# Kernel tuning notes

Measured on AMD Instinct MI355X. Metric: run time of the kernel, lower is better.

The kernel has to match this reference:

```python
import jax, jax.numpy as jnp
import numpy as np

NUM_HEADS = 1  # the module's reshape only type-checks for num_heads == 1 (see notes)


def setup_inputs() -> dict:
    key = jax.random.key(0)
    ks = jax.random.split(key, 9)
    B, S, H = 16, 4096, 512
    std = 0.02
    return {
        "x": jax.random.normal(ks[0], (B, S, H), dtype=jnp.float32),
        "Wq": jax.random.normal(ks[1], (H, H), dtype=jnp.float32) * std,
        "bq": jnp.zeros((H,), dtype=jnp.float32),
        "Wk": jax.random.normal(ks[2], (H, H), dtype=jnp.float32) * std,
        "bk": jnp.zeros((H,), dtype=jnp.float32),
        "Wv": jax.random.normal(ks[3], (H, H), dtype=jnp.float32) * std,
        "bv": jnp.zeros((H,), dtype=jnp.float32),
        "Wo": jax.random.normal(ks[4], (H, H), dtype=jnp.float32) * std,
        "bo": jnp.zeros((H,), dtype=jnp.float32),
    }


def reference(x, Wq, bq, Wk, bk, Wv, bv, Wo, bo):
    B, S, H = x.shape
    nh = NUM_HEADS
    hd = H // nh
    # Faithful to the torch code: view(B*nh, S, hd).transpose(1, 2) -> (G, hd, S)
    q = (x @ Wq + bq).reshape(B * nh, S, hd).transpose(0, 2, 1)  # (G, hd, S)
    k = (x @ Wk + bk).reshape(B * nh, S, hd).transpose(0, 2, 1)  # (G, hd, S)
    v = (x @ Wv + bv).reshape(B * nh, S, hd).transpose(0, 2, 1)  # (G, hd, S)
    # Attention matrix is over feature dims: (G, hd, hd), contraction over S
    scores = jnp.einsum('gds,ges->gde', q, k) / jnp.sqrt(jnp.float32(hd))
    attn = jax.nn.softmax(scores, axis=-1)                        # (G, hd, hd)
    attn_out = jnp.einsum('gde,ges->gds', attn, v)                # (G, hd, S)
    attn_out = attn_out.transpose(0, 2, 1)                        # (G, S, hd) == (B, S, H) for nh=1
    return attn_out @ Wo + bo
```

## Files before the change

kernel.cpp:

```cpp
#include <hip/hip_runtime.h>
#include <hip/hip_bf16.h>


typedef __attribute__((ext_vector_type(4))) float f32x4;
typedef __attribute__((ext_vector_type(8))) __bf16 bf16x8;
typedef __attribute__((ext_vector_type(4))) __bf16 bf16x4;

typedef __attribute__((address_space(1))) const void gconst_void;
typedef __attribute__((address_space(3))) void lds_void;

__device__ __forceinline__ void gload_lds16(const void* g, void* l) {
  __builtin_amdgcn_global_load_lds((gconst_void*)g, (lds_void*)l, 16, 0, 0);
}

__device__ __forceinline__ void cvt_hilo(float v, __bf16& h, __bf16& l) {
  h = (__bf16)v;
  l = (__bf16)(v - (float)h);
}

template <int MODE, int BMN>
__global__ __launch_bounds__(256) void gemm3p(
    const void* Ap, const void* ApLo,
    const void* Bp, const void* BpLo,
    float* __restrict__ C,
    int M, int N, int K,
    long long sAg, long long sBg, long long sCg,
    const float* bias, long long sBiasG,
    float alpha, int tri, int splitK)
{
  constexpr int LD = (MODE == 1) ? 64 : 72;
  constexpr int R = BMN / 32;
  __shared__ __align__(16) __bf16 sAhi[BMN * LD];
  __shared__ __align__(16) __bf16 sAlo[BMN * LD];
  __shared__ __align__(16) __bf16 sBhi[BMN * LD];
  __shared__ __align__(16) __bf16 sBlo[BMN * LD];

  const int t = threadIdx.x;
  const int g = blockIdx.z;
  int m0, n0, kBeg, kEnd;
  if (tri) {
    int p = blockIdx.x, bx = 0;
    while ((bx + 1) * (bx + 2) / 2 <= p) ++bx;
    int by = p - bx * (bx + 1) / 2;
    m0 = bx * BMN; n0 = by * BMN;
    int kLen = K / splitK;
    kBeg = blockIdx.y * kLen; kEnd = kBeg + kLen;
  } else {
    m0 = blockIdx.y * BMN; n0 = blockIdx.x * BMN;
    kBeg = 0; kEnd = K;
  }
  const int lane = t & 63;
  const int w = t >> 6, wm = w >> 1, wn = w & 1;
  const int lr = lane & 15, lg = lane >> 4;

  const f32x4 fzero = {0.f, 0.f, 0.f, 0.f};
  f32x4 acc[R][R];
#pragma unroll
  for (int i = 0; i < R; ++i)
#pragma unroll
    for (int j = 0; j < R; ++j) acc[i][j] = fzero;

  for (int k0 = kBeg; k0 < kEnd; k0 += 64) {
    __syncthreads();
    if constexpr (MODE == 1) {
      const __bf16* Ah = (const __bf16*)Ap + g * sAg;
      const __bf16* Al = (const __bf16*)ApLo + g * sAg;
      const __bf16* Bh = (const __bf16*)Bp + g * sBg;
      const __bf16* Bl = (const __bf16*)BpLo + g * sBg;
#pragma unroll
      for (int it = 0; it < BMN / 32; ++it) {
        int r = it * 32 + (t >> 3);
        int sl = (t & 7) ^ (r & 7);
        long long ea = (long long)(m0 + r) * K + k0 + sl * 8;
        long long eb = (long long)(n0 + r) * K + k0 + sl * 8;
        int dst = it * 4096 + (t >> 6) * 1024;
        gload_lds16(Ah + ea, (char*)sAhi + dst);
        gload_lds16(Al + ea, (char*)sAlo + dst);
        gload_lds16(Bh + eb, (char*)sBhi + dst);
        gload_lds16(Bl + eb, (char*)sBlo + dst);
      }
    } else {
      const float* A = (const float*)Ap + g * sAg;
      const float* B = (const float*)Bp + g * sBg;
      const int f = t & 15, r0 = t >> 4;
#pragma unroll
      for (int p = 0; p < BMN / 16; ++p) {
        int r = r0 + p * 16;
        float4 va = *(const float4*)(A + (long long)(m0 + r) * K + k0 + f * 4);
        float4 vb = *(const float4*)(B + (long long)(n0 + r) * K + k0 + f * 4);
        bf16x4 ah4, al4, bh4, bl4;
        __bf16 hh, ll;
        cvt_hilo(va.x, hh, ll); ah4[0] = hh; al4[0] = ll;
        cvt_hilo(va.y, hh, ll); ah4[1] = hh; al4[1] = ll;
        cvt_hilo(va.z, hh, ll); ah4[2] = hh; al4[2] = ll;
        cvt_hilo(va.w, hh, ll); ah4[3] = hh; al4[3] = ll;
        cvt_hilo(vb.x, hh, ll); bh4[0] = hh; bl4[0] = ll;
        cvt_hilo(vb.y, hh, ll); bh4[1] = hh; bl4[1] = ll;
        cvt_hilo(vb.z, hh, ll); bh4[2] = hh; bl4[2] = ll;
        cvt_hilo(vb.w, hh, ll); bh4[3] = hh; bl4[3] = ll;
        *(bf16x4*)&sAhi[r * LD + f * 4] = ah4;
        *(bf16x4*)&sAlo[r * LD + f * 4] = al4;
        *(bf16x4*)&sBhi[r * LD + f * 4] = bh4;
        *(bf16x4*)&sBlo[r * LD + f * 4] = bl4;
      }
    }
    __syncthreads();
#pragma unroll
    for (int ks = 0; ks < 2; ++ks) {
      bf16x8 ah[R], al[R], bh[R], bl[R];
#pragma unroll
      for (int i = 0; i < R; ++i) {
        int ra = wm * (BMN / 2) + i * 16 + lr;
        int rb = wn * (BMN / 2) + i * 16 + lr;
        int oa, ob;
        if constexpr (MODE == 1) {
          oa = ra * 64 + (((ks * 4 + lg) ^ (ra & 7)) * 8);
          ob = rb * 64 + (((ks * 4 + lg) ^ (rb & 7)) * 8);
        } else {
          oa = ra * LD + ks * 32 + lg * 8;
          ob = rb * LD + ks * 32 + lg * 8;
        }
        ah[i] = *(const bf16x8*)&sAhi[oa];
        al[i] = *(const bf16x8*)&sAlo[oa];
        bh[i] = *(const bf16x8*)&sBhi[ob];
        bl[i] = *(const bf16x8*)&sBlo[ob];
      }
#pragma unroll
      for (int i = 0; i < R; ++i)
#pragma unroll
        for (int j = 0; j < R; ++j) {
          acc[i][j] = __builtin_amdgcn_mfma_f32_16x16x32_bf16(ah[i], bh[j], acc[i][j], 0, 0, 0);
          acc[i][j] = __builtin_amdgcn_mfma_f32_16x16x32_bf16(ah[i], bl[j], acc[i][j], 0, 0, 0);
          acc[i][j] = __builtin_amdgcn_mfma_f32_16x16x32_bf16(al[i], bh[j], acc[i][j], 0, 0, 0);
        }
    }
  }

  float* Cg = C + g * sCg;
  const float* bg = bias ? bias + g * sBiasG : nullptr;
#pragma unroll
  for (int i = 0; i < R; ++i) {
    int row = m0 + wm * (BMN / 2) + i * 16 + lg * 4;
#pragma unroll
    for (int j = 0; j < R; ++j) {
      int col = n0 + wn * (BMN / 2) + j * 16 + lr;
      if (splitK > 1) {
#pragma unroll
        for (int q = 0; q < 4; ++q)
          atomicAdd(&Cg[(long long)(row + q) * N + col], acc[i][j][q] * alpha);
      } else {
        float bb = bg ? bg[col] : 0.0f;
#pragma unroll
        for (int q = 0; q < 4; ++q)
          Cg[(long long)(row + q) * N + col] = acc[i][j][q] * alpha + bb;
      }
    }
  }
}

__global__ __launch_bounds__(256) void transcvt_k(
    const float* __restrict__ x, __bf16* __restrict__ xTh, __bf16* __restrict__ xTl,
    float* __restrict__ ssum)
{
  __shared__ float tile[64][65];
  const int g = blockIdx.z, h0 = blockIdx.x * 64, s0 = blockIdx.y * 64;
  const int t = threadIdx.x, f = t & 15, r0 = t >> 4;
#pragma unroll
  for (int p = 0; p < 4; ++p) {
    int r = r0 + p * 16;
    float4 v = *(const float4*)(x + ((long long)g * 4096 + s0 + r) * 512 + h0 + f * 4);
    tile[f * 4 + 0][r] = v.x;
    tile[f * 4 + 1][r] = v.y;
    tile[f * 4 + 2][r] = v.z;
    tile[f * 4 + 3][r] = v.w;
  }
  __syncthreads();
  const int hr = t >> 2, sc = t & 3;
  long long ob = ((long long)g * 512 + h0 + hr) * 4096 + s0 + sc * 16;
  float csum = 0.f;
#pragma unroll
  for (int i4 = 0; i4 < 4; ++i4) {
    bf16x4 hv, lv;
#pragma unroll
    for (int q = 0; q < 4; ++q) {
      float vv = tile[hr][sc * 16 + i4 * 4 + q];
      csum += vv;
      __bf16 hh, ll;
      cvt_hilo(vv, hh, ll);
      hv[q] = hh; lv[q] = ll;
    }
    *(bf16x4*)(xTh + ob + i4 * 4) = hv;
    *(bf16x4*)(xTl + ob + i4 * 4) = lv;
  }
  csum += __shfl_xor(csum, 1);
  csum += __shfl_xor(csum, 2);
  if ((t & 3) == 0) atomicAdd(&ssum[g * 512 + h0 + hr], csum);
}

__global__ __launch_bounds__(256) void transp_k(
    const float* __restrict__ src, float* __restrict__ dst,
    int M, int N, long long sg, long long sgT, int triOnly)
{
  __shared__ float tile[64][65];
  const int g = blockIdx.z, n0 = blockIdx.x * 64, m0 = blockIdx.y * 64;
  if (triOnly && m0 <= n0) return;
  const int t = threadIdx.x, f = t & 15, r0 = t >> 4;
  const float* s = src + g * sg;
  float* d = dst + g * sgT;
#pragma unroll
  for (int p = 0; p < 4; ++p) {
    int r = r0 + p * 16;
    float4 v = *(const float4*)(s + (long long)(m0 + r) * N + n0 + f * 4);
    tile[f * 4 + 0][r] = v.x;
    tile[f * 4 + 1][r] = v.y;
    tile[f * 4 + 2][r] = v.z;
    tile[f * 4 + 3][r] = v.w;
  }
  __syncthreads();
  const int nr = t >> 2, mc = t & 3;
#pragma unroll
  for (int i4 = 0; i4 < 4; ++i4) {
    float4 o;
    o.x = tile[nr][mc * 16 + i4 * 4 + 0];
    o.y = tile[nr][mc * 16 + i4 * 4 + 1];
    o.z = tile[nr][mc * 16 + i4 * 4 + 2];
    o.w = tile[nr][mc * 16 + i4 * 4 + 3];
    *(float4*)(d + (long long)(n0 + nr) * M + m0 + mc * 16 + i4 * 4) = o;
  }
}

__global__ __launch_bounds__(256) void wtrans_k(
    const float* __restrict__ Wq, const float* __restrict__ Wk, const float* __restrict__ Wo,
    float* __restrict__ WqT, float* __restrict__ WkT, float* __restrict__ WoT)
{
  __shared__ float tile[64][65];
  const int z = blockIdx.z;
  const float* s = (z == 0) ? Wq : (z == 1) ? Wk : Wo;
  float* d = (z == 0) ? WqT : (z == 1) ? WkT : WoT;
  const int n0 = blockIdx.x * 64, m0 = blockIdx.y * 64;
  const int t = threadIdx.x, f = t & 15, r0 = t >> 4;
#pragma unroll
  for (int p = 0; p < 4; ++p) {
    int r = r0 + p * 16;
    float4 v = *(const float4*)(s + (long long)(m0 + r) * 512 + n0 + f * 4);
    tile[f * 4 + 0][r] = v.x;
    tile[f * 4 + 1][r] = v.y;
    tile[f * 4 + 2][r] = v.z;
    tile[f * 4 + 3][r] = v.w;
  }
  __syncthreads();
  const int nr = t >> 2, mc = t & 3;
#pragma unroll
  for (int i4 = 0; i4 < 4; ++i4) {
    float4 o;
    o.x = tile[nr][mc * 16 + i4 * 4 + 0];
    o.y = tile[nr][mc * 16 + i4 * 4 + 1];
    o.z = tile[nr][mc * 16 + i4 * 4 + 2];
    o.w = tile[nr][mc * 16 + i4 * 4 + 3];
    *(float4*)(d + (long long)(n0 + nr) * 512 + m0 + mc * 16 + i4 * 4) = o;
  }
}

__global__ __launch_bounds__(256) void cvt32_k(
    const float* __restrict__ src, __bf16* __restrict__ h, __bf16* __restrict__ l,
    long long n4)
{
  long long stride = (long long)gridDim.x * 256;
  for (long long i = blockIdx.x * 256LL + threadIdx.x; i < n4; i += stride) {
    float4 v = ((const float4*)src)[i];
    bf16x4 hv, lv;
    __bf16 hh, ll;
    cvt_hilo(v.x, hh, ll); hv[0] = hh; lv[0] = ll;
    cvt_hilo(v.y, hh, ll); hv[1] = hh; lv[1] = ll;
    cvt_hilo(v.z, hh, ll); hv[2] = hh; lv[2] = ll;
    cvt_hilo(v.w, hh, ll); hv[3] = hh; lv[3] = ll;
    *(bf16x4*)(h + i * 4) = hv;
    *(bf16x4*)(l + i * 4) = lv;
  }
}

__global__ __launch_bounds__(256) void rk_k(
    const float* __restrict__ ssum, const float* __restrict__ Wq, const float* __restrict__ Wk,
    float* __restrict__ rho, float* __restrict__ kap)
{
  const int g = blockIdx.y, d = blockIdx.x * 256 + threadIdx.x;
  float r = 0.f, k = 0.f;
  for (int f = 0; f < 512; ++f) {
    float s = ssum[g * 512 + f];
    r += s * Wq[f * 512 + d];
    k += s * Wk[f * 512 + d];
  }
  rho[g * 512 + d] = r;
  kap[g * 512 + d] = k;
}

__global__ __launch_bounds__(256) void softmax_k(
    float* __restrict__ SC, const float* __restrict__ rho, const float* __restrict__ kap,
    const float* __restrict__ bq, const float* __restrict__ bk, float alpha)
{
  const int rowid = blockIdx.x * 4 + (threadIdx.x >> 6);
  const int g = rowid >> 9, d = rowid & 511;
  const int l = threadIdx.x & 63;
  float* row = SC + (long long)rowid * 512;
  const float bqd = bq[d];
  const float rr = rho[g * 512 + d] + 4096.f * bqd;
  float4 z0 = *(float4*)(row + l * 8);
  float4 z1 = *(float4*)(row + l * 8 + 4);
  float4 bk0 = *(const float4*)(bk + l * 8);
  float4 bk1 = *(const float4*)(bk + l * 8 + 4);
  float4 kp0 = *(const float4*)(kap + g * 512 + l * 8);
  float4 kp1 = *(const float4*)(kap + g * 512 + l * 8 + 4);
  float z[8];
  z[0] = z0.x + alpha * (bqd * kp0.x + bk0.x * rr);
  z[1] = z0.y + alpha * (bqd * kp0.y + bk0.y * rr);
  z[2] = z0.z + alpha * (bqd * kp0.z + bk0.z * rr);
  z[3] = z0.w + alpha * (bqd * kp0.w + bk0.w * rr);
  z[4] = z1.x + alpha * (bqd * kp1.x + bk1.x * rr);
  z[5] = z1.y + alpha * (bqd * kp1.y + bk1.y * rr);
  z[6] = z1.z + alpha * (bqd * kp1.z + bk1.z * rr);
  z[7] = z1.w + alpha * (bqd * kp1.w + bk1.w * rr);
  float m = z[0];
#pragma unroll
  for (int j = 1; j < 8; ++j) m = fmaxf(m, z[j]);
  for (int o = 32; o; o >>= 1) m = fmaxf(m, __shfl_xor(m, o));
  float sum = 0.f;
#pragma unroll
  for (int j = 0; j < 8; ++j) { z[j] = __expf(z[j] - m); sum += z[j]; }
  for (int o = 32; o; o >>= 1) sum += __shfl_xor(sum, o);
  const float inv = 1.0f / sum;
  *(float4*)(row + l * 8)     = make_float4(z[0] * inv, z[1] * inv, z[2] * inv, z[3] * inv);
  *(float4*)(row + l * 8 + 4) = make_float4(z[4] * inv, z[5] * inv, z[6] * inv, z[7] * inv);
}

__global__ __launch_bounds__(256) void cvec_k(
    const float* __restrict__ Aat, const float* __restrict__ bv, const float* __restrict__ bo,
    float* __restrict__ c)
{
  const int g = blockIdx.z, h = blockIdx.x * 256 + threadIdx.x, eb = blockIdx.y;
  float p = (eb == 0) ? bo[h] : 0.f;
  for (int e = eb * 64; e < eb * 64 + 64; ++e)
    p += bv[e] * Aat[((long long)g * 512 + e) * 512 + h];
  atomicAdd(&c[g * 512 + h], p);
}

extern "C" void kernel_launch(void* const* d_in, const int* in_sizes, int n_in,
                              void* d_out, int out_size, void* d_ws, size_t ws_size,
                              hipStream_t stream) {
  (void)in_sizes; (void)n_in; (void)out_size; (void)ws_size;
  const float* x  = (const float*)d_in[0];
  const float* Wq = (const float*)d_in[1];
  const float* bq = (const float*)d_in[2];
  const float* Wk = (const float*)d_in[3];
  const float* bk = (const float*)d_in[4];
  const float* Wv = (const float*)d_in[5];
  const float* bv = (const float*)d_in[6];
  const float* Wo = (const float*)d_in[7];
  const float* bo = (const float*)d_in[8];
  float* out = (float*)d_out;

  char* ws = (char*)d_ws;
  __bf16* xTh = (__bf16*)(ws);
  __bf16* xTl = (__bf16*)(ws + 67108864);
  float* S1   = (float*)(ws + 134217728);
  float* S2   = (float*)(ws + 150994944);
  float* S3   = (float*)(ws + 167772160);
  float* WqT  = (float*)(ws + 184549376);
  float* WkT  = (float*)(ws + 185597952);
  float* WoT  = (float*)(ws + 186646528);
  float* ssum = (float*)(ws + 187695104);
  float* cbuf = (float*)(ws + 187695104 + 32768);
  float* rho  = (float*)(ws + 187695104 + 65536);
  float* kap  = (float*)(ws + 187695104 + 98304);

  __bf16* PThi = (__bf16*)S2;
  __bf16* PTlo = (__bf16*)((char*)S2 + 8388608);
  __bf16* xnh = xTh;
  __bf16* xnl = xTl;

  const long long SXT = 512LL * 4096;
  const long long SM  = 512LL * 512;
  const long long SX  = 4096LL * 512;
  const float alpha = 0.04419417382415922f;

  hipMemsetAsync(ssum, 0, 65536, stream);
  hipMemsetAsync(S1, 0, 16777216, stream);

  transcvt_k<<<dim3(8, 64, 16), 256, 0, stream>>>(x, xTh, xTl, ssum);
  wtrans_k<<<dim3(8, 8, 3), 256, 0, stream>>>(Wq, Wk, Wo, WqT, WkT, WoT);
  rk_k<<<dim3(2, 16), 256, 0, stream>>>(ssum, Wq, Wk, rho, kap);

  gemm3p<1, 128><<<dim3(10, 4, 16), 256, 0, stream>>>(
      xTh, xTl, xTh, xTl, S1, 512, 512, 4096, SXT, SXT, SM, nullptr, 0, 1.0f, 1, 4);
  transp_k<<<dim3(8, 8, 16), 256, 0, stream>>>(S1, S1, 512, 512, SM, SM, 1);

  gemm3p<0, 64><<<dim3(8, 8, 16), 256, 0, stream>>>(
      WkT, nullptr, S1, nullptr, S2, 512, 512, 512, 0, SM, SM, nullptr, 0, 1.0f, 0, 1);
  gemm3p<0, 64><<<dim3(8, 8, 16), 256, 0, stream>>>(
      WqT, nullptr, S2, nullptr, S3, 512, 512, 512, 0, SM, SM, nullptr, 0, alpha, 0, 1);
  softmax_k<<<2048, 256, 0, stream>>>(S3, rho, kap, bq, bk, alpha);
  transp_k<<<dim3(8, 8, 16), 256, 0, stream>>>(S3, S1, 512, 512, SM, SM, 0);
  gemm3p<0, 64><<<dim3(8, 8, 16), 256, 0, stream>>>(
      S1, nullptr, WoT, nullptr, S2, 512, 512, 512, SM, 0, SM, nullptr, 0, 1.0f, 0, 1);
  cvec_k<<<dim3(2, 8, 16), 256, 0, stream>>>(S2, bv, bo, cbuf);
  transp_k<<<dim3(8, 8, 16), 256, 0, stream>>>(S2, S3, 512, 512, SM, SM, 0);
  gemm3p<0, 64><<<dim3(8, 8, 16), 256, 0, stream>>>(
      S3, nullptr, Wv, nullptr, S1, 512, 512, 512, SM, 0, SM, nullptr, 0, 1.0f, 0, 1);

  cvt32_k<<<2048, 256, 0, stream>>>(S1, PThi, PTlo, 16LL * 512 * 512 / 4);
  cvt32_k<<<2048, 256, 0, stream>>>(x, xnh, xnl, 16LL * 4096 * 512 / 4);

  gemm3p<1, 128><<<dim3(4, 32, 16), 256, 0, stream>>>(
      xnh, xnl, PThi, PTlo, out, 4096, 512, 512, SX, SM, SX, cbuf, 512, 1.0f, 0, 1);
}
```

Measured before the change: 717.3 us.

## Fuse conversions, transposes and bias vector into neighbouring kernels; shrink MODE1 K-tile

```diff
diff --git a/kernel.cpp b/kernel.cpp
--- a/kernel.cpp
+++ b/kernel.cpp
@@ -22,18 +22,22 @@
 __global__ __launch_bounds__(256) void gemm3p(
     const void* Ap, const void* ApLo,
     const void* Bp, const void* BpLo,
-    float* __restrict__ C,
+    float* __restrict__ C, __bf16* __restrict__ Cbh, __bf16* __restrict__ Cbl,
     int M, int N, int K,
     long long sAg, long long sBg, long long sCg,
     const float* bias, long long sBiasG,
-    float alpha, int tri, int splitK)
-{
-  constexpr int LD = (MODE == 1) ? 64 : 72;
+    float alpha, int tri, int splitK, int tepi)
+{
+  constexpr int LD = (MODE == 1) ? 32 : 72;
+  constexpr int BK = (MODE == 1) ? 32 : 64;
+  constexpr int KS = BK / 32;
   constexpr int R = BMN / 32;
-  __shared__ __align__(16) __bf16 sAhi[BMN * LD];
-  __shared__ __align__(16) __bf16 sAlo[BMN * LD];
-  __shared__ __align__(16) __bf16 sBhi[BMN * LD];
-  __shared__ __align__(16) __bf16 sBlo[BMN * LD];
+  __shared__ __align__(16) char smem[4 * BMN * LD * 2];
+  __bf16* sAhi = (__bf16*)smem;
+  __bf16* sAlo = sAhi + BMN * LD;
+  __bf16* sBhi = sAlo + BMN * LD;
+  __bf16* sBlo = sBhi + BMN * LD;
+  float* tpose = (float*)smem;
 
   const int t = threadIdx.x;
   const int g = blockIdx.z;
@@ -60,7 +64,7 @@
 #pragma unroll
     for (int j = 0; j < R; ++j) acc[i][j] = fzero;
 
-  for (int k0 = kBeg; k0 < kEnd; k0 += 64) {
+  for (int k0 = kBeg; k0 < kEnd; k0 += BK) {
     __syncthreads();
     if constexpr (MODE == 1) {
       const __bf16* Ah = (const __bf16*)Ap + g * sAg;
@@ -68,12 +72,12 @@
       const __bf16* Bh = (const __bf16*)Bp + g * sBg;
       const __bf16* Bl = (const __bf16*)BpLo + g * sBg;
 #pragma unroll
-      for (int it = 0; it < BMN / 32; ++it) {
-        int r = it * 32 + (t >> 3);
-        int sl = (t & 7) ^ (r & 7);
+      for (int half = 0; half < 2; ++half) {
+        int r = half * 64 + (t >> 2);
+        int sl = (t & 3) ^ (r & 3);
         long long ea = (long long)(m0 + r) * K + k0 + sl * 8;
         long long eb = (long long)(n0 + r) * K + k0 + sl * 8;
-        int dst = it * 4096 + (t >> 6) * 1024;
+        int dst = half * 4096 + (t >> 6) * 1024;
         gload_lds16(Ah + ea, (char*)sAhi + dst);
         gload_lds16(Al + ea, (char*)sAlo + dst);
         gload_lds16(Bh + eb, (char*)sBhi + dst);
@@ -106,7 +110,7 @@
     }
     __syncthreads();
 #pragma unroll
-    for (int ks = 0; ks < 2; ++ks) {
+    for (int ks = 0; ks < KS; ++ks) {
       bf16x8 ah[R], al[R], bh[R], bl[R];
 #pragma unroll
       for (int i = 0; i < R; ++i) {
@@ -114,8 +118,8 @@
         int rb = wn * (BMN / 2) + i * 16 + lr;
         int oa, ob;
         if constexpr (MODE == 1) {
-          oa = ra * 64 + (((ks * 4 + lg) ^ (ra & 7)) * 8);
-          ob = rb * 64 + (((ks * 4 + lg) ^ (rb & 7)) * 8);
+          oa = ra * 32 + ((lg ^ (ra & 3)) * 8);
+          ob = rb * 32 + ((lg ^ (rb & 3)) * 8);
         } else {
           oa = ra * LD + ks * 32 + lg * 8;
           ob = rb * LD + ks * 32 + lg * 8;
@@ -136,6 +140,55 @@
     }
   }
 
+  if (tepi) {
+    __syncthreads();
+#pragma unroll
+    for (int i = 0; i < R; ++i) {
+      int rowl = wm * (BMN / 2) + i * 16 + lg * 4;
+#pragma unroll
+      for (int j = 0; j < R; ++j) {
+        int coll = wn * (BMN / 2) + j * 16 + lr;
+#pragma unroll
+        for (int q = 0; q < 4; ++q)
+          tpose[(rowl + q) * 65 + coll] = acc[i][j][q] * alpha;
+      }
+    }
+    __syncthreads();
+    float* Cg = C + g * sCg;
+    const int nr = t >> 2, mc = t & 3;
+#pragma unroll
+    for (int i4 = 0; i4 < 4; ++i4) {
+      float4 o;
+      o.x = tpose[(mc * 16 + i4 * 4 + 0) * 65 + nr];
+      o.y = tpose[(mc * 16 + i4 * 4 + 1) * 65 + nr];
+      o.z = tpose[(mc * 16 + i4 * 4 + 2) * 65 + nr];
+      o.w = tpose[(mc * 16 + i4 * 4 + 3) * 65 + nr];
+      *(float4*)&Cg[(long long)(n0 + nr) * M + m0 + mc * 16 + i4 * 4] = o;
+    }
+    return;
+  }
+
+  if (Cbh) {
+    __bf16* Ch = Cbh + g * sCg;
+    __bf16* Cl2 = Cbl + g * sCg;
+#pragma unroll
+    for (int i = 0; i < R; ++i) {
+      int row = m0 + wm * (BMN / 2) + i * 16 + lg * 4;
+#pragma unroll
+      for (int j = 0; j < R; ++j) {
+        int col = n0 + wn * (BMN / 2) + j * 16 + lr;
+#pragma unroll
+        for (int q = 0; q < 4; ++q) {
+          __bf16 hh, ll;
+          cvt_hilo(acc[i][j][q] * alpha, hh, ll);
+          Ch[(long long)(row + q) * N + col] = hh;
+          Cl2[(long long)(row + q) * N + col] = ll;
+        }
+      }
+    }
+    return;
+  }
+
   float* Cg = C + g * sCg;
   const float* bg = bias ? bias + g * sBiasG : nullptr;
 #pragma unroll
@@ -160,7 +213,7 @@
 
 __global__ __launch_bounds__(256) void transcvt_k(
     const float* __restrict__ x, __bf16* __restrict__ xTh, __bf16* __restrict__ xTl,
-    float* __restrict__ ssum)
+    __bf16* __restrict__ xh, __bf16* __restrict__ xl, float* __restrict__ ssum)
 {
   __shared__ float tile[64][65];
   const int g = blockIdx.z, h0 = blockIdx.x * 64, s0 = blockIdx.y * 64;
@@ -168,7 +221,18 @@
 #pragma unroll
   for (int p = 0; p < 4; ++p) {
     int r = r0 + p * 16;
-    float4 v = *(const float4*)(x + ((long long)g * 4096 + s0 + r) * 512 + h0 + f * 4);
+    long long ib = ((long long)g * 4096 + s0 + r) * 512 + h0 + f * 4;
+    float4 v = *(const float4*)(x + ib);
+    if (xh) {
+      bf16x4 hv, lv;
+      __bf16 hh, ll;
+      cvt_hilo(v.x, hh, ll); hv[0] = hh; lv[0] = ll;
+      cvt_hilo(v.y, hh, ll); hv[1] = hh; lv[1] = ll;
+      cvt_hilo(v.z, hh, ll); hv[2] = hh; lv[2] = ll;
+      cvt_hilo(v.w, hh, ll); hv[3] = hh; lv[3] = ll;
+      *(bf16x4*)(xh + ib) = hv;
+      *(bf16x4*)(xl + ib) = lv;
+    }
     tile[f * 4 + 0][r] = v.x;
     tile[f * 4 + 1][r] = v.y;
     tile[f * 4 + 2][r] = v.z;
@@ -296,7 +360,8 @@
 
 __global__ __launch_bounds__(256) void softmax_k(
     float* __restrict__ SC, const float* __restrict__ rho, const float* __restrict__ kap,
-    const float* __restrict__ bq, const float* __restrict__ bk, float alpha)
+    const float* __restrict__ bq, const float* __restrict__ bk, const float* __restrict__ bv,
+    float* __restrict__ avb, float alpha)
 {
   const int rowid = blockIdx.x * 4 + (threadIdx.x >> 6);
   const int g = rowid >> 9, d = rowid & 511;
@@ -330,23 +395,28 @@
   const float inv = 1.0f / sum;
   *(float4*)(row + l * 8)     = make_float4(z[0] * inv, z[1] * inv, z[2] * inv, z[3] * inv);
   *(float4*)(row + l * 8 + 4) = make_float4(z[4] * inv, z[5] * inv, z[6] * inv, z[7] * inv);
-}
-
-__global__ __launch_bounds__(256) void cvec_k(
-    const float* __restrict__ Aat, const float* __restrict__ bv, const float* __restrict__ bo,
+  float4 bv0 = *(const float4*)(bv + l * 8);
+  float4 bv1 = *(const float4*)(bv + l * 8 + 4);
+  float av = z[0] * bv0.x + z[1] * bv0.y + z[2] * bv0.z + z[3] * bv0.w +
+             z[4] * bv1.x + z[5] * bv1.y + z[6] * bv1.z + z[7] * bv1.w;
+  for (int o = 32; o; o >>= 1) av += __shfl_xor(av, o);
+  if (l == 0) avb[g * 512 + d] = av * inv;
+}
+
+__global__ __launch_bounds__(256) void cvec2_k(
+    const float* __restrict__ avb, const float* __restrict__ Wo, const float* __restrict__ bo,
     float* __restrict__ c)
 {
-  const int g = blockIdx.z, h = blockIdx.x * 256 + threadIdx.x, eb = blockIdx.y;
-  float p = (eb == 0) ? bo[h] : 0.f;
-  for (int e = eb * 64; e < eb * 64 + 64; ++e)
-    p += bv[e] * Aat[((long long)g * 512 + e) * 512 + h];
-  atomicAdd(&c[g * 512 + h], p);
+  const int g = blockIdx.y, h = blockIdx.x * 256 + threadIdx.x;
+  float p = bo[h];
+  for (int d = 0; d < 512; ++d) p += avb[g * 512 + d] * Wo[d * 512 + h];
+  c[g * 512 + h] = p;
 }
 
 extern "C" void kernel_launch(void* const* d_in, const int* in_sizes, int n_in,
                               void* d_out, int out_size, void* d_ws, size_t ws_size,
                               hipStream_t stream) {
-  (void)in_sizes; (void)n_in; (void)out_size; (void)ws_size;
+  (void)in_sizes; (void)n_in; (void)out_size;
   const float* x  = (const float*)d_in[0];
   const float* Wq = (const float*)d_in[1];
   const float* bq = (const float*)d_in[2];
@@ -359,56 +429,78 @@
   float* out = (float*)d_out;
 
   char* ws = (char*)d_ws;
-  __bf16* xTh = (__bf16*)(ws);
-  __bf16* xTl = (__bf16*)(ws + 67108864);
-  float* S1   = (float*)(ws + 134217728);
-  float* S2   = (float*)(ws + 150994944);
-  float* S3   = (float*)(ws + 167772160);
-  float* WqT  = (float*)(ws + 184549376);
-  float* WkT  = (float*)(ws + 185597952);
-  float* WoT  = (float*)(ws + 186646528);
-  float* ssum = (float*)(ws + 187695104);
-  float* cbuf = (float*)(ws + 187695104 + 32768);
-  float* rho  = (float*)(ws + 187695104 + 65536);
-  float* kap  = (float*)(ws + 187695104 + 98304);
+  const long long MB = 1048576;
+  const bool big = ws_size >= (size_t)(324 * MB);
+
+  __bf16* xTh; __bf16* xTl; __bf16* xh; __bf16* xl;
+  float *S1, *S2, *S3, *WqT, *WkT, *WoT, *ssum, *avb, *cbuf, *rho, *kap;
+  if (big) {
+    xTh = (__bf16*)(ws);               xTl = (__bf16*)(ws + 64 * MB);
+    xh  = (__bf16*)(ws + 128 * MB);    xl  = (__bf16*)(ws + 192 * MB);
+    S1  = (float*)(ws + 256 * MB);
+    S2  = (float*)(ws + 272 * MB);
+    S3  = (float*)(ws + 288 * MB);
+    WqT = (float*)(ws + 304 * MB);
+    WkT = (float*)(ws + 305 * MB);
+    WoT = (float*)(ws + 306 * MB);
+    ssum = (float*)(ws + 307 * MB);
+  } else {
+    xTh = (__bf16*)(ws);               xTl = (__bf16*)(ws + 64 * MB);
+    xh  = xTh;                         xl  = xTl;
+    S1  = (float*)(ws + 128 * MB);
+    S2  = (float*)(ws + 144 * MB);
+    S3  = (float*)(ws + 160 * MB);
+    WqT = (float*)(ws + 176 * MB);
+    WkT = (float*)(ws + 177 * MB);
+    WoT = (float*)(ws + 178 * MB);
+    ssum = (float*)(ws + 179 * MB);
+  }
+  avb  = ssum + 8192;
+  cbuf = ssum + 16384;
+  rho  = ssum + 24576;
+  kap  = ssum + 32768;
 
   __bf16* PThi = (__bf16*)S2;
-  __bf16* PTlo = (__bf16*)((char*)S2 + 8388608);
-  __bf16* xnh = xTh;
-  __bf16* xnl = xTl;
+  __bf16* PTlo = PThi + 16LL * 512 * 512;
 
   const long long SXT = 512LL * 4096;
   const long long SM  = 512LL * 512;
   const long long SX  = 4096LL * 512;
   const float alpha = 0.04419417382415922f;
 
-  hipMemsetAsync(ssum, 0, 65536, stream);
+  hipMemsetAsync(ssum, 0, 32768, stream);
   hipMemsetAsync(S1, 0, 16777216, stream);
 
-  transcvt_k<<<dim3(8, 64, 16), 256, 0, stream>>>(x, xTh, xTl, ssum);
+  transcvt_k<<<dim3(8, 64, 16), 256, 0, stream>>>(
+      x, xTh, xTl, big ? xh : nullptr, big ? xl : nullptr, ssum);
   wtrans_k<<<dim3(8, 8, 3), 256, 0, stream>>>(Wq, Wk, Wo, WqT, WkT, WoT);
   rk_k<<<dim3(2, 16), 256, 0, stream>>>(ssum, Wq, Wk, rho, kap);
 
   gemm3p<1, 128><<<dim3(10, 4, 16), 256, 0, stream>>>(
-      xTh, xTl, xTh, xTl, S1, 512, 512, 4096, SXT, SXT, SM, nullptr, 0, 1.0f, 1, 4);
+      xTh, xTl, xTh, xTl, S1, nullptr, nullptr, 512, 512, 4096,
+      SXT, SXT, SM, nullptr, 0, 1.0f, 1, 4, 0);
   transp_k<<<dim3(8, 8, 16), 256, 0, stream>>>(S1, S1, 512, 512, SM, SM, 1);
 
   gemm3p<0, 64><<<dim3(8, 8, 16), 256, 0, stream>>>(
-      WkT, nullptr, S1, nullptr, S2, 512, 512, 512, 0, SM, SM, nullptr, 0, 1.0f, 0, 1);
+      WkT, nullptr, S1, nullptr, S2, nullptr, nullptr, 512, 512, 512,
+      0, SM, SM, nullptr, 0, 1.0f, 0, 1, 0);
   gemm3p<0, 64><<<dim3(8, 8, 16), 256, 0, stream>>>(
-      WqT, nullptr, S2, nullptr, S3, 512, 512, 512, 0, SM, SM, nullptr, 0, alpha, 0, 1);
-  softmax_k<<<2048, 256, 0, stream>>>(S3, rho, kap, bq, bk, alpha);
-  transp_k<<<dim3(8, 8, 16), 256, 0, stream>>>(S3, S1, 512, 512, SM, SM, 0);
+      WqT, nullptr, S2, nullptr, S3, nullptr, nullptr, 512, 512, 512,
+      0, SM, SM, nullptr, 0, alpha, 0, 1, 0);
+  softmax_k<<<2048, 256, 0, stream>>>(S3, rho, kap, bq, bk, bv, avb, alpha);
+  cvec2_k<<<dim3(2, 16), 256, 0, stream>>>(avb, Wo, bo, cbuf);
+
   gemm3p<0, 64><<<dim3(8, 8, 16), 256, 0, stream>>>(
-      S1, nullptr, WoT, nullptr, S2, 512, 512, 512, SM, 0, SM, nullptr, 0, 1.0f, 0, 1);
-  cvec_k<<<dim3(2, 8, 16), 256, 0, stream>>>(S2, bv, bo, cbuf);
-  transp_k<<<dim3(8, 8, 16), 256, 0, stream>>>(S2, S3, 512, 512, SM, SM, 0);
+      S3, nullptr, Wv, nullptr, S1, nullptr, nullptr, 512, 512, 512,
+      SM, 0, SM, nullptr, 0, 1.0f, 0, 1, 1);
   gemm3p<0, 64><<<dim3(8, 8, 16), 256, 0, stream>>>(
-      S3, nullptr, Wv, nullptr, S1, 512, 512, 512, SM, 0, SM, nullptr, 0, 1.0f, 0, 1);
-
-  cvt32_k<<<2048, 256, 0, stream>>>(S1, PThi, PTlo, 16LL * 512 * 512 / 4);
-  cvt32_k<<<2048, 256, 0, stream>>>(x, xnh, xnl, 16LL * 4096 * 512 / 4);
+      WoT, nullptr, S1, nullptr, nullptr, PThi, PTlo, 512, 512, 512,
+      0, SM, SM, nullptr, 0, 1.0f, 0, 1, 0);
+
+  if (!big)
+    cvt32_k<<<2048, 256, 0, stream>>>(x, xh, xl, 16LL * 4096 * 512 / 4);
 
   gemm3p<1, 128><<<dim3(4, 32, 16), 256, 0, stream>>>(
-      xnh, xnl, PThi, PTlo, out, 4096, 512, 512, SX, SM, SX, cbuf, 512, 1.0f, 0, 1);
-}
+      xh, xl, PThi, PTlo, out, nullptr, nullptr, 4096, 512, 512,
+      SX, SM, SX, cbuf, 512, 1.0f, 0, 1, 0);
+}
```

Result: slower. 741.9 us (+3.4%).
